# Kernel tuning notes

Hardware: AMD Instinct MI355X
Metric: run time of the kernel (lower is better)

The kernel has to match this reference:

```python
import jax, jax.numpy as jnp
import numpy as np


def setup_inputs() -> dict:
    key = jax.random.key(0)
    ks = jax.random.split(key, 5)
    B, T, C = 4, 2048, 768
    return {
        "x": jax.random.normal(ks[0], (B, T, C), dtype=jnp.float32),
        "w_attn": jax.random.normal(ks[1], (C, 3 * C), dtype=jnp.float32) * 0.02,
        "b_attn": jax.random.normal(ks[2], (3 * C,), dtype=jnp.float32) * 0.02,
        "w_proj": jax.random.normal(ks[3], (C, C), dtype=jnp.float32) * 0.02,
        "b_proj": jax.random.normal(ks[4], (C,), dtype=jnp.float32) * 0.02,
    }


N_HEAD = 8
SOFTMAX_EPS = 1e-6  # the CUDA kernel divides by (sum + 1e-6)


def reference(x, w_attn, b_attn, w_proj, b_proj):
    B, T, C = x.shape
    H = N_HEAD
    hs = C // H
    scale = 1.0 / np.sqrt(hs).astype(np.float32)

    qkv = x @ w_attn + b_attn                      # [B, T, 3C]
    q, k, v = jnp.split(qkv, 3, axis=-1)           # each [B, T, C]
    # reorder to [B, H, T, hs] (matches fused_reorder_qkv)
    def heads(t):
        return t.reshape(B, T, H, hs).transpose(0, 2, 1, 3)
    q, k, v = heads(q), heads(k), heads(v)

    att = jnp.einsum('bhqd,bhkd->bhqk', q, k) * scale
    causal = jnp.tril(jnp.ones((T, T), dtype=bool))  # [T, T]
    att = jnp.where(causal, att, -jnp.inf)
    # kernel softmax: exp(x - max) / (sum + eps)
    m = jnp.max(att, axis=-1, keepdims=True)
    e = jnp.exp(att - m)
    att = e / (jnp.sum(e, axis=-1, keepdims=True) + SOFTMAX_EPS)

    y = jnp.einsum('bhqk,bhkd->bhqd', att, v)      # [B, H, T, hs]
    y = y.transpose(0, 2, 1, 3).reshape(B, T, C)   # fused_reorder_output
    return y @ w_proj + b_proj
```

## Files before the change

kernel.cpp:

```cpp
#include <hip/hip_runtime.h>

constexpr int Bn = 4;
constexpr int Tn = 2048;
constexpr int Cn = 768;
constexpr int Hn = 8;
constexpr int HSn = 96;
constexpr int MR = Bn * Tn;
constexpr int NQKV = 3 * Cn;

typedef __attribute__((ext_vector_type(8))) short bf16x8;
typedef __attribute__((ext_vector_type(4))) float f32x4;

__device__ inline short f2bf(float f) {
  union { float f; unsigned u; } cv; cv.f = f;
  unsigned u = cv.u;
  u += 0x7fffu + ((u >> 16) & 1u);
  return (short)(u >> 16);
}

__device__ inline void gload_lds16(const short* g, short* l) {
  __builtin_amdgcn_global_load_lds(
      (const __attribute__((address_space(1))) unsigned*)g,
      (__attribute__((address_space(3))) unsigned*)l, 16, 0, 0);
}

__global__ __launch_bounds__(256) void cvt_bf16(const float* __restrict__ in,
                                                short* __restrict__ out) {
  const size_t i = ((size_t)blockIdx.x * 256 + threadIdx.x) * 8;
  float4 a = *(const float4*)(in + i);
  float4 b = *(const float4*)(in + i + 4);
  bf16x8 o;
  o[0] = f2bf(a.x); o[1] = f2bf(a.y); o[2] = f2bf(a.z); o[3] = f2bf(a.w);
  o[4] = f2bf(b.x); o[5] = f2bf(b.y); o[6] = f2bf(b.z); o[7] = f2bf(b.w);
  *(bf16x8*)(out + i) = o;
}

__global__ __launch_bounds__(256) void transpose_bf16(
    const float* __restrict__ W, short* __restrict__ Wt, int K, int N) {
  __shared__ float t[32][33];
  const int n0 = blockIdx.x * 32, k0 = blockIdx.y * 32;
  const int tx = threadIdx.x & 31, ty = threadIdx.x >> 5;
  #pragma unroll
  for (int i = 0; i < 32; i += 8)
    t[ty + i][tx] = W[(size_t)(k0 + ty + i) * N + n0 + tx];
  __syncthreads();
  #pragma unroll
  for (int i = 0; i < 32; i += 8)
    Wt[(size_t)(n0 + ty + i) * K + k0 + tx] = f2bf(t[tx][ty + i]);
}

__global__ __launch_bounds__(256) void build_vt(
    const short* __restrict__ qkv, short* __restrict__ vt) {
  __shared__ short Vl[64][104];
  const int blk = blockIdx.x;
  const int kt = blk & 31, bh = blk >> 5;
  const int b = bh >> 3, h = bh & 7;
  const int k0 = kt * 64;
  const int tid = threadIdx.x;

  #pragma unroll
  for (int i = tid; i < 768; i += 256) {
    const int r = i / 12, ch = i % 12;
    *(bf16x8*)&Vl[r][ch * 8] = *(const bf16x8*)(
        qkv + ((size_t)(b * Tn + k0 + r)) * NQKV + 2 * Cn + h * HSn + ch * 8);
  }
  __syncthreads();
  #pragma unroll
  for (int i = tid; i < 768; i += 256) {
    const int d = i >> 3, w = i & 7;
    bf16x8 o;
    #pragma unroll
    for (int u = 0; u < 8; ++u) o[u] = Vl[w * 8 + u][d];
    *(bf16x8*)(vt + (size_t)blk * 6144 + d * 64 + w * 8) = o;
  }
}

template <bool BF16OUT>
__global__ __launch_bounds__(256) void gemm_mfma(
    const short* __restrict__ A, const short* __restrict__ Bt,
    const float* __restrict__ bias, float* __restrict__ Cf,
    short* __restrict__ Cb, int M, int N, int K, int nxTiles,
    int scale_cols, float scale) {
  __shared__ short As[128 * 32];
  __shared__ short Bs[128 * 32];

  const int cpx = gridDim.x >> 3;
  const int lin = blockIdx.x;
  const int remap = (lin & 7) * cpx + (lin >> 3);
  const int bxt = remap % nxTiles, byt = remap / nxTiles;

  const int tid  = threadIdx.x;
  const int wave = tid >> 6, lane = tid & 63;
  const int bm = byt * 128, bn = bxt * 128;
  const int wr = wave >> 1, wc = wave & 1;
  const int g = lane >> 4, c = lane & 15;

  f32x4 acc[4][4] = {};

  for (int k0 = 0; k0 < K; k0 += 32) {
    __syncthreads();
    #pragma unroll
    for (int cc = 0; cc < 2; ++cc) {
      const int chunkbase = (wave * 2 + cc) * 64;
      const int chunk = chunkbase + lane;
      const int row = chunk >> 2, col16 = chunk & 3;
      gload_lds16(A + (size_t)(bm + row) * K + k0 + col16 * 8,
                  &As[chunkbase * 8]);
      gload_lds16(Bt + (size_t)(bn + row) * K + k0 + col16 * 8,
                  &Bs[chunkbase * 8]);
    }
    __syncthreads();

    bf16x8 af[4], bfr[4];
    #pragma unroll
    for (int m = 0; m < 4; ++m)
      af[m] = *(const bf16x8*)&As[(wr * 64 + m * 16 + c) * 32 + g * 8];
    #pragma unroll
    for (int n = 0; n < 4; ++n)
      bfr[n] = *(const bf16x8*)&Bs[(wc * 64 + n * 16 + c) * 32 + g * 8];
    #pragma unroll
    for (int m = 0; m < 4; ++m)
      #pragma unroll
      for (int n = 0; n < 4; ++n)
        acc[m][n] = __builtin_amdgcn_mfma_f32_16x16x32_bf16(af[m], bfr[n], acc[m][n], 0, 0, 0);
  }

  #pragma unroll
  for (int n = 0; n < 4; ++n) {
    const int col = bn + wc * 64 + n * 16 + c;
    const float bs = bias[col];
    const float sc = (BF16OUT && col < scale_cols) ? scale : 1.f;
    #pragma unroll
    for (int m = 0; m < 4; ++m) {
      #pragma unroll
      for (int r = 0; r < 4; ++r) {
        const int row = bm + wr * 64 + m * 16 + g * 4 + r;
        const float v = acc[m][n][r] + bs;
        if (BF16OUT) Cb[(size_t)row * N + col] = f2bf(v * sc);
        else         Cf[(size_t)row * N + col] = v;
      }
    }
  }
}

__global__ __launch_bounds__(256) void attn_mfma(
    const short* __restrict__ qkv, const short* __restrict__ vt,
    short* __restrict__ y) {
  __shared__ short Ksub[2][6144];
  __shared__ short Pl[4][16][72];

  const int bid = blockIdx.x;
  const int xcd = bid & 7, jj = bid >> 3;
  const int p = xcd + 8 * (jj >> 4);
  const int bx = jj & 15;
  const int b = p >> 3, h = p & 7;

  const int tid  = threadIdx.x;
  const int wave = tid >> 6;
  const int lane = tid & 63;
  const int g = lane >> 4;
  const int c = lane & 15;

  const int klane = ((c >> 2) * 6 + (g >> 1)) * 64 + (c & 3) * 16 + (g & 1) * 8;
  const int voff  = c * 64 + g * 8;
  const short* vtb = vt + (size_t)((b * 8 + h) * 32) * 6144;

  for (int phase = 0; phase < 2; ++phase) {
    const int qt = phase ? (31 - bx) : bx;
    const int q0 = qt * 64 + wave * 16;

    bf16x8 qf[3];
    {
      const size_t qb = ((size_t)(b * Tn + q0 + c)) * NQKV + h * HSn;
      #pragma unroll
      for (int kk = 0; kk < 3; ++kk)
        qf[kk] = *(const bf16x8*)(qkv + qb + kk * 32 + g * 8);
    }

    const short* kap[3];
    #pragma unroll
    for (int j = 0; j < 3; ++j) {
      const int ci = (j * 4 + wave) * 64 + lane;
      const int s = ci >> 3;
      const int kb = s / 6, db = s - kb * 6;
      const int r = kb * 4 + ((ci & 7) >> 1);
      const int d0 = db * 16 + (ci & 1) * 8;
      kap[j] = qkv + ((size_t)(b * Tn + r)) * NQKV + Cn + h * HSn + d0;
    }
    #pragma unroll
    for (int j = 0; j < 3; ++j) {
      gload_lds16(kap[j], &Ksub[0][(j * 4 + wave) * 512]);
      kap[j] += 64 * NQKV;
    }

    f32x4 yacc[6] = {};
    float mrow[4] = {-1e30f, -1e30f, -1e30f, -1e30f};
    float lrow[4] = {};
    int buf = 0;

    for (int kt = 0; kt <= qt; ++kt) {
      __syncthreads();

      const short* vtile = vtb + (size_t)kt * 6144 + voff;
      bf16x8 vf[12];
      #pragma unroll
      for (int ks = 0; ks < 2; ++ks)
        #pragma unroll
        for (int dt = 0; dt < 6; ++dt)
          vf[ks * 6 + dt] = *(const bf16x8*)(vtile + dt * 1024 + ks * 32);

      if (kt < qt) {
        #pragma unroll
        for (int j = 0; j < 3; ++j) {
          gload_lds16(kap[j], &Ksub[buf ^ 1][(j * 4 + wave) * 512]);
          kap[j] += 64 * NQKV;
        }
      }

      const int k0 = kt * 64;

      f32x4 s[4] = {};
      __builtin_amdgcn_s_setprio(1);
      #pragma unroll
      for (int kk = 0; kk < 3; ++kk) {
        #pragma unroll
        for (int t = 0; t < 4; ++t) {
          bf16x8 kf = *(const bf16x8*)&Ksub[buf][klane + (24 * t + 2 * kk) * 64];
          s[t] = __builtin_amdgcn_mfma_f32_16x16x32_bf16(qf[kk], kf, s[t], 0, 0, 0);
        }
      }
      __builtin_amdgcn_s_setprio(0);
      if (kt == qt) {
        #pragma unroll
        for (int t = 0; t < 4; ++t)
          #pragma unroll
          for (int r = 0; r < 4; ++r)
            if (k0 + 16 * t + c > q0 + 4 * g + r) s[t][r] = -1e30f;
      }

      #pragma unroll
      for (int r = 0; r < 4; ++r) {
        float mx = fmaxf(fmaxf(s[0][r], s[1][r]), fmaxf(s[2][r], s[3][r]));
        mx = fmaxf(mx, __shfl_xor(mx, 1));
        mx = fmaxf(mx, __shfl_xor(mx, 2));
        mx = fmaxf(mx, __shfl_xor(mx, 4));
        mx = fmaxf(mx, __shfl_xor(mx, 8));
        if (mx > mrow[r] + 8.f) {
          const float corr = exp2f(mrow[r] - mx);
          lrow[r] *= corr;
          #pragma unroll
          for (int dt = 0; dt < 6; ++dt) yacc[dt][r] *= corr;
          mrow[r] = mx;
        }
        float ls = 0.f;
        #pragma unroll
        for (int t = 0; t < 4; ++t) {
          const float pv = exp2f(s[t][r] - mrow[r]);
          ls += pv;
          Pl[wave][4 * g + r][16 * t + c] = f2bf(pv);
        }
        lrow[r] += ls;
      }

      __builtin_amdgcn_s_setprio(1);
      #pragma unroll
      for (int ks = 0; ks < 2; ++ks) {
        bf16x8 pf = *(const bf16x8*)&Pl[wave][c][ks * 32 + g * 8];
        #pragma unroll
        for (int dt = 0; dt < 6; ++dt)
          yacc[dt] = __builtin_amdgcn_mfma_f32_16x16x32_bf16(pf, vf[ks * 6 + dt], yacc[dt], 0, 0, 0);
      }
      __builtin_amdgcn_s_setprio(0);

      buf ^= 1;
    }

    #pragma unroll
    for (int r = 0; r < 4; ++r) {
      float v = lrow[r];
      v += __shfl_xor(v, 1);
      v += __shfl_xor(v, 2);
      v += __shfl_xor(v, 4);
      v += __shfl_xor(v, 8);
      lrow[r] = 1.f / (v + 1e-6f);
    }
    #pragma unroll
    for (int dt = 0; dt < 6; ++dt)
      #pragma unroll
      for (int r = 0; r < 4; ++r)
        y[((size_t)(b * Tn + q0 + 4 * g + r)) * Cn + h * HSn + 16 * dt + c] =
            f2bf(yacc[dt][r] * lrow[r]);
  }
}

extern "C" void kernel_launch(void* const* d_in, const int* in_sizes, int n_in,
                              void* d_out, int out_size, void* d_ws, size_t ws_size,
                              hipStream_t stream) {
  const float* x      = (const float*)d_in[0];
  const float* w_attn = (const float*)d_in[1];
  const float* b_attn = (const float*)d_in[2];
  const float* w_proj = (const float*)d_in[3];
  const float* b_proj = (const float*)d_in[4];
  float* out = (float*)d_out;

  size_t off = 0;
  short* qkv = (short*)((char*)d_ws + off); off += (size_t)MR * NQKV * 2;
  short* xb  = (short*)((char*)d_ws + off); off += (size_t)MR * Cn * 2;
  short* yb  = (short*)((char*)d_ws + off); off += (size_t)MR * Cn * 2;
  short* wat = (short*)((char*)d_ws + off); off += (size_t)Cn * NQKV * 2;
  short* wpt = (short*)((char*)d_ws + off); off += (size_t)Cn * Cn * 2;
  if (ws_size < off) return;
  short* vt = xb;

  const float scale = 0.102062072615966f * 1.4426950408889634f;

  cvt_bf16<<<(MR * Cn) / (256 * 8), 256, 0, stream>>>(x, xb);
  transpose_bf16<<<dim3(NQKV / 32, Cn / 32), 256, 0, stream>>>(w_attn, wat, Cn, NQKV);
  transpose_bf16<<<dim3(Cn / 32, Cn / 32), 256, 0, stream>>>(w_proj, wpt, Cn, Cn);

  gemm_mfma<true><<<(NQKV / 128) * (MR / 128), 256, 0, stream>>>(
      xb, wat, b_attn, nullptr, qkv, MR, NQKV, Cn, NQKV / 128, Cn, scale);

  build_vt<<<Bn * Hn * 32, 256, 0, stream>>>(qkv, vt);

  attn_mfma<<<512, 256, 0, stream>>>(qkv, vt, yb);

  gemm_mfma<false><<<(Cn / 128) * (MR / 128), 256, 0, stream>>>(
      yb, wpt, b_proj, out, nullptr, MR, Cn, Cn, Cn / 128, 0, 1.f);
}
```

Before: 200.8 us.

## Split attention KV range across two wave groups and merge partial softmax

The attention kernel now launches 512 threads per block. The KV tiles for each query tile are split between two groups of four waves, and each group keeps its own double-buffered K staging. The second group writes its partial output, running max and sum into shared memory, and the first group combines them with rescaling before writing the result. This is meant to double the parallelism per query tile and shorten the sequential KV loop, at the cost of more LDS use, extra barriers, the merge step, and possible occupancy limits.

```diff
diff --git a/kernel.cpp b/kernel.cpp
--- a/kernel.cpp
+++ b/kernel.cpp
@@ -143,11 +143,13 @@
   }
 }
 
-__global__ __launch_bounds__(256) void attn_mfma(
+__global__ __launch_bounds__(512, 4) void attn_mfma(
     const short* __restrict__ qkv, const short* __restrict__ vt,
     short* __restrict__ y) {
-  __shared__ short Ksub[2][6144];
-  __shared__ short Pl[4][16][72];
+  __shared__ short Ksub[2][2][6144];
+  __shared__ short Pl[8][16][72];
+  float* mergeY  = (float*)&Ksub[1][0][0];
+  float* mergeML = (float*)&Pl[0][0][0];
 
   const int bid = blockIdx.x;
   const int xcd = bid & 7, jj = bid >> 3;
@@ -157,6 +159,8 @@
 
   const int tid  = threadIdx.x;
   const int wave = tid >> 6;
+  const int grp  = wave >> 2;
+  const int wg   = wave & 3;
   const int lane = tid & 63;
   const int g = lane >> 4;
   const int c = lane & 15;
@@ -167,7 +171,10 @@
 
   for (int phase = 0; phase < 2; ++phase) {
     const int qt = phase ? (31 - bx) : bx;
-    const int q0 = qt * 64 + wave * 16;
+    const int n  = (qt + 2) >> 1;
+    const int tbase = grp ? n : 0;
+    const int tend  = grp ? (qt + 1) : n;
+    const int q0 = qt * 64 + wg * 16;
 
     bf16x8 qf[3];
     {
@@ -180,17 +187,19 @@
     const short* kap[3];
     #pragma unroll
     for (int j = 0; j < 3; ++j) {
-      const int ci = (j * 4 + wave) * 64 + lane;
+      const int ci = (j * 4 + wg) * 64 + lane;
       const int s = ci >> 3;
       const int kb = s / 6, db = s - kb * 6;
       const int r = kb * 4 + ((ci & 7) >> 1);
       const int d0 = db * 16 + (ci & 1) * 8;
-      kap[j] = qkv + ((size_t)(b * Tn + r)) * NQKV + Cn + h * HSn + d0;
-    }
-    #pragma unroll
-    for (int j = 0; j < 3; ++j) {
-      gload_lds16(kap[j], &Ksub[0][(j * 4 + wave) * 512]);
-      kap[j] += 64 * NQKV;
+      kap[j] = qkv + ((size_t)(b * Tn + tbase * 64 + r)) * NQKV + Cn + h * HSn + d0;
+    }
+    if (tbase < tend) {
+      #pragma unroll
+      for (int j = 0; j < 3; ++j) {
+        gload_lds16(kap[j], &Ksub[grp][0][(j * 4 + wg) * 512]);
+        kap[j] += 64 * NQKV;
+      }
     }
 
     f32x4 yacc[6] = {};
@@ -198,79 +207,84 @@
     float lrow[4] = {};
     int buf = 0;
 
-    for (int kt = 0; kt <= qt; ++kt) {
+    for (int it = 0; it < n; ++it) {
       __syncthreads();
-
-      const short* vtile = vtb + (size_t)kt * 6144 + voff;
+      const int kt = tbase + it;
+      const bool act = kt < tend;
+
       bf16x8 vf[12];
-      #pragma unroll
-      for (int ks = 0; ks < 2; ++ks)
-        #pragma unroll
-        for (int dt = 0; dt < 6; ++dt)
-          vf[ks * 6 + dt] = *(const bf16x8*)(vtile + dt * 1024 + ks * 32);
-
-      if (kt < qt) {
+      if (act) {
+        const short* vtile = vtb + (size_t)kt * 6144 + voff;
+        #pragma unroll
+        for (int ks = 0; ks < 2; ++ks)
+          #pragma unroll
+          for (int dt = 0; dt < 6; ++dt)
+            vf[ks * 6 + dt] = *(const bf16x8*)(vtile + dt * 1024 + ks * 32);
+      }
+
+      if (kt + 1 < tend) {
         #pragma unroll
         for (int j = 0; j < 3; ++j) {
-          gload_lds16(kap[j], &Ksub[buf ^ 1][(j * 4 + wave) * 512]);
+          gload_lds16(kap[j], &Ksub[grp][buf ^ 1][(j * 4 + wg) * 512]);
           kap[j] += 64 * NQKV;
         }
       }
 
-      const int k0 = kt * 64;
-
-      f32x4 s[4] = {};
-      __builtin_amdgcn_s_setprio(1);
-      #pragma unroll
-      for (int kk = 0; kk < 3; ++kk) {
-        #pragma unroll
-        for (int t = 0; t < 4; ++t) {
-          bf16x8 kf = *(const bf16x8*)&Ksub[buf][klane + (24 * t + 2 * kk) * 64];
-          s[t] = __builtin_amdgcn_mfma_f32_16x16x32_bf16(qf[kk], kf, s[t], 0, 0, 0);
-        }
-      }
-      __builtin_amdgcn_s_setprio(0);
-      if (kt == qt) {
-        #pragma unroll
-        for (int t = 0; t < 4; ++t)
-          #pragma unroll
-          for (int r = 0; r < 4; ++r)
-            if (k0 + 16 * t + c > q0 + 4 * g + r) s[t][r] = -1e30f;
-      }
-
-      #pragma unroll
-      for (int r = 0; r < 4; ++r) {
-        float mx = fmaxf(fmaxf(s[0][r], s[1][r]), fmaxf(s[2][r], s[3][r]));
-        mx = fmaxf(mx, __shfl_xor(mx, 1));
-        mx = fmaxf(mx, __shfl_xor(mx, 2));
-        mx = fmaxf(mx, __shfl_xor(mx, 4));
-        mx = fmaxf(mx, __shfl_xor(mx, 8));
-        if (mx > mrow[r] + 8.f) {
-          const float corr = exp2f(mrow[r] - mx);
-          lrow[r] *= corr;
-          #pragma unroll
-          for (int dt = 0; dt < 6; ++dt) yacc[dt][r] *= corr;
-          mrow[r] = mx;
-        }
-        float ls = 0.f;
-        #pragma unroll
-        for (int t = 0; t < 4; ++t) {
-          const float pv = exp2f(s[t][r] - mrow[r]);
-          ls += pv;
-          Pl[wave][4 * g + r][16 * t + c] = f2bf(pv);
-        }
-        lrow[r] += ls;
-      }
-
-      __builtin_amdgcn_s_setprio(1);
-      #pragma unroll
-      for (int ks = 0; ks < 2; ++ks) {
-        bf16x8 pf = *(const bf16x8*)&Pl[wave][c][ks * 32 + g * 8];
-        #pragma unroll
-        for (int dt = 0; dt < 6; ++dt)
-          yacc[dt] = __builtin_amdgcn_mfma_f32_16x16x32_bf16(pf, vf[ks * 6 + dt], yacc[dt], 0, 0, 0);
-      }
-      __builtin_amdgcn_s_setprio(0);
+      if (act) {
+        const int k0 = kt * 64;
+        f32x4 s[4] = {};
+        __builtin_amdgcn_s_setprio(1);
+        #pragma unroll
+        for (int kk = 0; kk < 3; ++kk) {
+          #pragma unroll
+          for (int t = 0; t < 4; ++t) {
+            bf16x8 kf = *(const bf16x8*)&Ksub[grp][buf][klane + (24 * t + 2 * kk) * 64];
+            s[t] = __builtin_amdgcn_mfma_f32_16x16x32_bf16(qf[kk], kf, s[t], 0, 0, 0);
+          }
+        }
+        __builtin_amdgcn_s_setprio(0);
+        if (kt == qt) {
+          #pragma unroll
+          for (int t = 0; t < 4; ++t)
+            #pragma unroll
+            for (int r = 0; r < 4; ++r)
+              if (k0 + 16 * t + c > q0 + 4 * g + r) s[t][r] = -1e30f;
+        }
+
+        #pragma unroll
+        for (int r = 0; r < 4; ++r) {
+          float mx = fmaxf(fmaxf(s[0][r], s[1][r]), fmaxf(s[2][r], s[3][r]));
+          mx = fmaxf(mx, __shfl_xor(mx, 1));
+          mx = fmaxf(mx, __shfl_xor(mx, 2));
+          mx = fmaxf(mx, __shfl_xor(mx, 4));
+          mx = fmaxf(mx, __shfl_xor(mx, 8));
+          if (mx > mrow[r] + 8.f) {
+            const float corr = exp2f(mrow[r] - mx);
+            lrow[r] *= corr;
+            #pragma unroll
+            for (int dt = 0; dt < 6; ++dt) yacc[dt][r] *= corr;
+            mrow[r] = mx;
+          }
+          float ls = 0.f;
+          #pragma unroll
+          for (int t = 0; t < 4; ++t) {
+            const float pv = exp2f(s[t][r] - mrow[r]);
+            ls += pv;
+            Pl[wave][4 * g + r][16 * t + c] = f2bf(pv);
+          }
+          lrow[r] += ls;
+        }
+
+        __builtin_amdgcn_s_setprio(1);
+        #pragma unroll
+        for (int ks = 0; ks < 2; ++ks) {
+          bf16x8 pf = *(const bf16x8*)&Pl[wave][c][ks * 32 + g * 8];
+          #pragma unroll
+          for (int dt = 0; dt < 6; ++dt)
+            yacc[dt] = __builtin_amdgcn_mfma_f32_16x16x32_bf16(pf, vf[ks * 6 + dt], yacc[dt], 0, 0, 0);
+        }
+        __builtin_amdgcn_s_setprio(0);
+      }
 
       buf ^= 1;
     }
@@ -282,14 +296,42 @@
       v += __shfl_xor(v, 2);
       v += __shfl_xor(v, 4);
       v += __shfl_xor(v, 8);
-      lrow[r] = 1.f / (v + 1e-6f);
-    }
-    #pragma unroll
-    for (int dt = 0; dt < 6; ++dt)
-      #pragma unroll
-      for (int r = 0; r < 4; ++r)
-        y[((size_t)(b * Tn + q0 + 4 * g + r)) * Cn + h * HSn + 16 * dt + c] =
-            f2bf(yacc[dt][r] * lrow[r]);
+      lrow[r] = v;
+    }
+
+    __syncthreads();
+    if (grp == 1) {
+      #pragma unroll
+      for (int r = 0; r < 4; ++r) {
+        const int row = wg * 16 + 4 * g + r;
+        #pragma unroll
+        for (int dt = 0; dt < 6; ++dt)
+          mergeY[row * 96 + 16 * dt + c] = yacc[dt][r];
+        if (c == 0) {
+          mergeML[row * 2 + 0] = mrow[r];
+          mergeML[row * 2 + 1] = lrow[r];
+        }
+      }
+    }
+    __syncthreads();
+    if (grp == 0) {
+      #pragma unroll
+      for (int r = 0; r < 4; ++r) {
+        const int row = wg * 16 + 4 * g + r;
+        const float mB = mergeML[row * 2 + 0];
+        const float lB = mergeML[row * 2 + 1];
+        const float m  = fmaxf(mrow[r], mB);
+        const float sA = exp2f(mrow[r] - m);
+        const float sB = exp2f(mB - m);
+        const float inv = 1.f / (lrow[r] * sA + lB * sB + 1e-6f);
+        #pragma unroll
+        for (int dt = 0; dt < 6; ++dt) {
+          const float yv = (yacc[dt][r] * sA + mergeY[row * 96 + 16 * dt + c] * sB) * inv;
+          y[((size_t)(b * Tn + q0 + 4 * g + r)) * Cn + h * HSn + 16 * dt + c] = f2bf(yv);
+        }
+      }
+    }
+    __syncthreads();
   }
 }
 
@@ -323,7 +365,7 @@
 
   build_vt<<<Bn * Hn * 32, 256, 0, stream>>>(qkv, vt);
 
-  attn_mfma<<<512, 256, 0, stream>>>(qkv, vt, yb);
+  attn_mfma<<<512, 512, 0, stream>>>(qkv, vt, yb);
 
   gemm_mfma<false><<<(Cn / 128) * (MR / 128), 256, 0, stream>>>(
       yb, wpt, b_proj, out, nullptr, MR, Cn, Cn, Cn / 128, 0, 1.f);
```

After: 234.8 us. +16.9%, slower.
